# Optimization experiments

Measured on AMD Instinct MI355X. Metric: run time of the kernel, lower is better.

The kernel has to match this reference:

```python
import jax, jax.numpy as jnp
import numpy as np

NEG = -1000000000.0

def setup_inputs() -> dict:
    key = jax.random.key(0)
    k1, k2, k3, k4 = jax.random.split(key, 4)
    B, Sq, Sk, D = 8, 2048, 2048, 1024
    query = jax.random.normal(k1, (B, Sq, D), dtype=jnp.float32)
    memories = jax.random.normal(k2, (B, Sk, D), dtype=jnp.float32)
    mask = jax.random.randint(k3, (B, Sq, Sk), 0, 2).astype(jnp.int32)
    W = jax.random.normal(k4, (D, D), dtype=jnp.float32) * (1.0 / np.sqrt(D))
    b = jnp.zeros((D,), dtype=jnp.float32)
    return {"query": query, "memories": memories, "mask": mask, "W": W, "b": b}

def reference(query, memories, mask, W, b):
    # linear projection: nn.Linear applies x @ W^T + b
    q = jnp.einsum('bsd,od->bso', query, W) + b
    add_mask = (1.0 - mask.astype(q.dtype)) * NEG
    # [B,Sq,Sk] attention logits
    attn_logits = jnp.einsum('bqd,bkd->bqk', q, memories) + add_mask
    attn_weights = jax.nn.softmax(attn_logits, axis=-1)
    attn_outputs = jnp.einsum('bqk,bkd->bqd', attn_weights, memories)
    return attn_outputs
```

## Files before the change

kernel.cpp:

```cpp
#include <hip/hip_runtime.h>


typedef __attribute__((ext_vector_type(8))) _Float16 f16x8;
typedef __attribute__((ext_vector_type(4))) float f32x4;
typedef unsigned short u16;
typedef unsigned int u32;

#define B_ 8
#define SQL 2048
#define SKL 2048
#define DD 1024
#define NEGC -1000000000.0f

static __device__ __forceinline__ u16 f2h(float x) {
  _Float16 h = (_Float16)x;
  return __builtin_bit_cast(u16, h);
}
static __device__ __forceinline__ float h2f(u16 v) {
  return (float)__builtin_bit_cast(_Float16, v);
}
static __device__ __forceinline__ void gload16(const void* g, void* l) {
  __builtin_amdgcn_global_load_lds((const __attribute__((address_space(1))) u32*)g,
                                   (__attribute__((address_space(3))) u32*)l, 16, 0, 0);
}

__global__ __launch_bounds__(256) void cvt16_k(const float* __restrict__ in,
                                               u16* __restrict__ out, long n) {
  long i = ((long)blockIdx.x * 256 + threadIdx.x) * 8;
  long stride = (long)gridDim.x * 256 * 8;
  for (; i < n; i += stride) {
    float4 v0 = *(const float4*)(in + i);
    float4 v1 = *(const float4*)(in + i + 4);
    ushort4 o0 = make_ushort4(f2h(v0.x), f2h(v0.y), f2h(v0.z), f2h(v0.w));
    ushort4 o1 = make_ushort4(f2h(v1.x), f2h(v1.y), f2h(v1.z), f2h(v1.w));
    *(ushort4*)(out + i) = o0;
    *(ushort4*)(out + i + 4) = o1;
  }
}

__global__ __launch_bounds__(256) void split16_k(const float* __restrict__ in,
                                                 u16* __restrict__ hi, u16* __restrict__ lo,
                                                 long n) {
  long i = ((long)blockIdx.x * 256 + threadIdx.x) * 4;
  long stride = (long)gridDim.x * 256 * 4;
  for (; i < n; i += stride) {
    float4 v = *(const float4*)(in + i);
    u16 h0 = f2h(v.x), h1 = f2h(v.y), h2 = f2h(v.z), h3 = f2h(v.w);
    *(ushort4*)(hi + i) = make_ushort4(h0, h1, h2, h3);
    *(ushort4*)(lo + i) = make_ushort4(f2h(v.x - h2f(h0)), f2h(v.y - h2f(h1)),
                                       f2h(v.z - h2f(h2)), f2h(v.w - h2f(h3)));
  }
}

__global__ __launch_bounds__(256) void split_mem16_k(const float* __restrict__ in,
                                                     u16* __restrict__ hi,
                                                     u16* __restrict__ trn) {
  __shared__ u16 t[64][65];
  long bo = (long)blockIdx.z * SKL * DD;
  int r0 = blockIdx.y * 64, c0 = blockIdx.x * 64;
  int tr = threadIdx.x / 16, tc4 = (threadIdx.x % 16) * 4;
#pragma unroll
  for (int i = 0; i < 4; ++i) {
    int r = tr + i * 16;
    long idx = bo + (long)(r0 + r) * DD + c0 + tc4;
    float4 v = *(const float4*)(in + idx);
    u16 h0 = f2h(v.x), h1 = f2h(v.y), h2 = f2h(v.z), h3 = f2h(v.w);
    *(ushort4*)(hi + idx) = make_ushort4(h0, h1, h2, h3);
    t[r][tc4 + 0] = h0; t[r][tc4 + 1] = h1; t[r][tc4 + 2] = h2; t[r][tc4 + 3] = h3;
  }
  __syncthreads();
#pragma unroll
  for (int i = 0; i < 4; ++i) {
    int c = tr + i * 16;
    ushort4 v = make_ushort4(t[tc4 + 0][c], t[tc4 + 1][c], t[tc4 + 2][c], t[tc4 + 3][c]);
    *(ushort4*)(trn + bo + (long)(c0 + c) * SKL + r0 + tc4) = v;
  }
}

template <int TERMS, int OUTMODE, bool BIAS>
__global__ __launch_bounds__(256, 2) void gemm_f16(
    const u16* __restrict__ Ah,
    const u16* __restrict__ Bh, const u16* __restrict__ Bl,
    const float* __restrict__ bias,
    void* __restrict__ C0,
    int N, int K, long batchA, long batchB, long batchC) {
  constexpr int RWB = (TERMS == 2) ? 128 : 64;
  __shared__ u16 lA[128 * 64];
  __shared__ u16 lB[128 * RWB];

  const int nx = gridDim.x;
  int i0 = blockIdx.y * nx + blockIdx.x;
  int nwg = nx * gridDim.y;
  int j = (i0 & 7) * (nwg >> 3) + (i0 >> 3);
  const int bx = j % nx, by = j / nx;

  const int bz = blockIdx.z;
  const u16* pAh = Ah + (long)bz * batchA;
  const u16* pBh = Bh + (long)bz * batchB;
  const u16* pBl = (TERMS == 2) ? Bl : nullptr;

  const int tid = threadIdx.x;
  const int l = tid & 63, w = tid >> 6;
  const int wr = w >> 1, wc = w & 1;
  const long am0 = (long)by * 128;
  const long bn0 = (long)bx * 128;

  f32x4 acc[4][4];
#pragma unroll
  for (int i = 0; i < 4; ++i)
#pragma unroll
    for (int j2 = 0; j2 < 4; ++j2) {
      f32x4 z = {0.f, 0.f, 0.f, 0.f};
      acc[i][j2] = z;
    }

  const int lrow = l & 15, lch = l >> 4;

  for (int k0 = 0; k0 < K; k0 += 64) {
    __syncthreads();
#pragma unroll
    for (int i = 0; i < 4; ++i) {
      int row = i * 32 + (tid >> 3);
      int cc = (tid & 7) ^ (row & 7);
      gload16(pAh + (am0 + row) * K + k0 + cc * 8, &lA[row * 64 + (tid & 7) * 8]);
    }
    if (TERMS == 2) {
#pragma unroll
      for (int i = 0; i < 8; ++i) {
        int row = i * 16 + (tid >> 4);
        int s = tid & 15;
        int cc = s ^ (row & 15);
        const u16* src = (cc < 8) ? (pBh + (bn0 + row) * K + k0 + cc * 8)
                                  : (pBl + (bn0 + row) * K + k0 + (cc - 8) * 8);
        gload16(src, &lB[row * 128 + s * 8]);
      }
    } else {
#pragma unroll
      for (int i = 0; i < 4; ++i) {
        int row = i * 32 + (tid >> 3);
        int cc = (tid & 7) ^ (row & 7);
        gload16(pBh + (bn0 + row) * K + k0 + cc * 8, &lB[row * 64 + (tid & 7) * 8]);
      }
    }
    __syncthreads();

#pragma unroll
    for (int kk = 0; kk < 2; ++kk) {
      if (TERMS == 2) {
        f16x8 ah[4], bh[4], bl_[4];
#pragma unroll
        for (int f = 0; f < 4; ++f) {
          int ra = wr * 64 + f * 16 + lrow;
          int rb = wc * 64 + f * 16 + lrow;
          int c = kk * 4 + lch;
          ah[f] = *(const f16x8*)&lA[ra * 64 + (c ^ (ra & 7)) * 8];
          bh[f] = *(const f16x8*)&lB[rb * 128 + (c ^ (rb & 15)) * 8];
          bl_[f] = *(const f16x8*)&lB[rb * 128 + ((8 + c) ^ (rb & 15)) * 8];
        }
#pragma unroll
        for (int mf = 0; mf < 4; ++mf)
#pragma unroll
          for (int nf = 0; nf < 4; ++nf) {
            acc[mf][nf] = __builtin_amdgcn_mfma_f32_16x16x32_f16(ah[mf], bh[nf], acc[mf][nf], 0, 0, 0);
            acc[mf][nf] = __builtin_amdgcn_mfma_f32_16x16x32_f16(ah[mf], bl_[nf], acc[mf][nf], 0, 0, 0);
          }
      } else {
        f16x8 ah[4], bh[4];
#pragma unroll
        for (int f = 0; f < 4; ++f) {
          int ra = wr * 64 + f * 16 + lrow;
          int rb = wc * 64 + f * 16 + lrow;
          int c = kk * 4 + lch;
          ah[f] = *(const f16x8*)&lA[ra * 64 + (c ^ (ra & 7)) * 8];
          bh[f] = *(const f16x8*)&lB[rb * 64 + (c ^ (rb & 7)) * 8];
        }
#pragma unroll
        for (int mf = 0; mf < 4; ++mf)
#pragma unroll
          for (int nf = 0; nf < 4; ++nf)
            acc[mf][nf] = __builtin_amdgcn_mfma_f32_16x16x32_f16(ah[mf], bh[nf], acc[mf][nf], 0, 0, 0);
      }
    }
  }

#pragma unroll
  for (int mf = 0; mf < 4; ++mf)
#pragma unroll
    for (int nf = 0; nf < 4; ++nf)
#pragma unroll
      for (int r = 0; r < 4; ++r) {
        long row = am0 + wr * 64 + mf * 16 + (l >> 4) * 4 + r;
        long col = bn0 + wc * 64 + nf * 16 + (l & 15);
        float v = acc[mf][nf][r];
        if (BIAS) v += bias[col];
        long idx = (long)bz * batchC + row * N + col;
        if (OUTMODE == 0) ((float*)C0)[idx] = v;
        else              ((u16*)C0)[idx] = f2h(v);
      }
}

__global__ __launch_bounds__(256) void softmax16_k(const float* __restrict__ S,
                                                   const int* __restrict__ M,
                                                   u16* __restrict__ P) {
  long row = blockIdx.x;
  const float* s = S + row * SKL;
  const int* m = M + row * SKL;
  u16* p = P + row * SKL;
  int t = threadIdx.x;
  float x[8];
#pragma unroll
  for (int j = 0; j < 2; ++j) {
    float4 v = *(const float4*)(s + t * 8 + j * 4);
    int4 q = *(const int4*)(m + t * 8 + j * 4);
    x[j * 4 + 0] = q.x ? v.x : v.x + NEGC;
    x[j * 4 + 1] = q.y ? v.y : v.y + NEGC;
    x[j * 4 + 2] = q.z ? v.z : v.z + NEGC;
    x[j * 4 + 3] = q.w ? v.w : v.w + NEGC;
  }
  float mx = x[0];
#pragma unroll
  for (int j = 1; j < 8; ++j) mx = fmaxf(mx, x[j]);
#pragma unroll
  for (int o = 32; o >= 1; o >>= 1) mx = fmaxf(mx, __shfl_xor(mx, o, 64));
  __shared__ float red[8];
  if ((t & 63) == 0) red[t >> 6] = mx;
  __syncthreads();
  mx = fmaxf(fmaxf(red[0], red[1]), fmaxf(red[2], red[3]));
  float e[8], sum = 0.f;
#pragma unroll
  for (int j = 0; j < 8; ++j) { e[j] = __expf(x[j] - mx); sum += e[j]; }
#pragma unroll
  for (int o = 32; o >= 1; o >>= 1) sum += __shfl_xor(sum, o, 64);
  if ((t & 63) == 0) red[4 + (t >> 6)] = sum;
  __syncthreads();
  float inv = 1.f / (red[4] + red[5] + red[6] + red[7]);
  ushort4 o0 = make_ushort4(f2h(e[0] * inv), f2h(e[1] * inv), f2h(e[2] * inv), f2h(e[3] * inv));
  ushort4 o1 = make_ushort4(f2h(e[4] * inv), f2h(e[5] * inv), f2h(e[6] * inv), f2h(e[7] * inv));
  *(ushort4*)(p + t * 8) = o0;
  *(ushort4*)(p + t * 8 + 4) = o1;
}

extern "C" void kernel_launch(void* const* d_in, const int* in_sizes, int n_in,
                              void* d_out, int out_size, void* d_ws, size_t ws_size,
                              hipStream_t stream) {
  const float* query = (const float*)d_in[0];
  const float* mem = (const float*)d_in[1];
  const int* mask = (const int*)d_in[2];
  const float* Wm = (const float*)d_in[3];
  const float* bias = (const float*)d_in[4];
  float* out = (float*)d_out;

  const long nQ = (long)B_ * SQL * DD;
  const long nW = (long)DD * DD;
  const long nS = (long)B_ * SQL * SKL;

  char* ws = (char*)d_ws;
  u16* q16 = (u16*)ws; ws += nQ * 2;
  u16* memh = (u16*)ws; ws += nQ * 2;
  u16* memT = (u16*)ws; ws += nQ * 2;
  u16* q1 = (u16*)ws; ws += nQ * 2;
  u16* wh = (u16*)ws; ws += nW * 2;
  u16* wl = (u16*)ws; ws += nW * 2;
  float* S = (float*)ws; ws += nS * 4;
  u16* P = q16;

  cvt16_k<<<2048, 256, 0, stream>>>(query, q16, nQ);
  split16_k<<<512, 256, 0, stream>>>(Wm, wh, wl, nW);
  split_mem16_k<<<dim3(DD / 64, SKL / 64, B_), 256, 0, stream>>>(mem, memh, memT);

  gemm_f16<2, 1, true><<<dim3(DD / 128, (B_ * SQL) / 128, 1), 256, 0, stream>>>(
      q16, wh, wl, bias, q1, DD, DD, 0, 0, 0);
  gemm_f16<1, 0, false><<<dim3(SKL / 128, SQL / 128, B_), 256, 0, stream>>>(
      q1, memh, nullptr, nullptr, S, SKL, DD,
      (long)SQL * DD, (long)SKL * DD, (long)SQL * SKL);
  softmax16_k<<<B_ * SQL, 256, 0, stream>>>(S, mask, P);
  gemm_f16<1, 0, false><<<dim3(DD / 128, SQL / 128, B_), 256, 0, stream>>>(
      P, memT, nullptr, nullptr, out, DD, SKL,
      (long)SQL * SKL, (long)DD * SKL, (long)SQL * DD);
}
```

Before: 353.9 us.

## Double-buffer LDS tiles in single-term f16 GEMM to overlap loads with MFMA

For the TERMS==1 GEMM variant, LDS tiles are doubled so the next k-tile's global-to-LDS loads are issued before computing the current tile. Partial vmcnt waits and raw s_barrier calls with sched barriers replace the two __syncthreads per iteration. This hides global load latency behind MFMA work. The cost is double the LDS for this variant, which may limit the two-blocks-per-CU occupancy. The two-term path is unchanged.

```diff
diff --git a/kernel.cpp b/kernel.cpp
--- a/kernel.cpp
+++ b/kernel.cpp
@@ -84,9 +84,10 @@
     const float* __restrict__ bias,
     void* __restrict__ C0,
     int N, int K, long batchA, long batchB, long batchC) {
+  constexpr int NBUF = (TERMS == 1) ? 2 : 1;
   constexpr int RWB = (TERMS == 2) ? 128 : 64;
-  __shared__ u16 lA[128 * 64];
-  __shared__ u16 lB[128 * RWB];
+  __shared__ u16 lA[NBUF][128 * 64];
+  __shared__ u16 lB[NBUF][128 * RWB];
 
   const int nx = gridDim.x;
   int i0 = blockIdx.y * nx + blockIdx.x;
@@ -116,15 +117,64 @@
 
   const int lrow = l & 15, lch = l >> 4;
 
-  for (int k0 = 0; k0 < K; k0 += 64) {
-    __syncthreads();
-#pragma unroll
-    for (int i = 0; i < 4; ++i) {
-      int row = i * 32 + (tid >> 3);
-      int cc = (tid & 7) ^ (row & 7);
-      gload16(pAh + (am0 + row) * K + k0 + cc * 8, &lA[row * 64 + (tid & 7) * 8]);
+  if constexpr (TERMS == 1) {
+    auto STAGE = [&](int buf, int k0) {
+#pragma unroll
+      for (int i = 0; i < 4; ++i) {
+        int row = i * 32 + (tid >> 3);
+        int cc = (tid & 7) ^ (row & 7);
+        gload16(pAh + (am0 + row) * K + k0 + cc * 8, &lA[buf][row * 64 + (tid & 7) * 8]);
+        gload16(pBh + (bn0 + row) * K + k0 + cc * 8, &lB[buf][row * 64 + (tid & 7) * 8]);
+      }
+    };
+    auto COMPUTE = [&](int buf) {
+#pragma unroll
+      for (int kk = 0; kk < 2; ++kk) {
+        f16x8 ah[4], bh[4];
+#pragma unroll
+        for (int f = 0; f < 4; ++f) {
+          int ra = wr * 64 + f * 16 + lrow;
+          int rb = wc * 64 + f * 16 + lrow;
+          int c = kk * 4 + lch;
+          ah[f] = *(const f16x8*)&lA[buf][ra * 64 + (c ^ (ra & 7)) * 8];
+          bh[f] = *(const f16x8*)&lB[buf][rb * 64 + (c ^ (rb & 7)) * 8];
+        }
+#pragma unroll
+        for (int mf = 0; mf < 4; ++mf)
+#pragma unroll
+          for (int nf = 0; nf < 4; ++nf)
+            acc[mf][nf] = __builtin_amdgcn_mfma_f32_16x16x32_f16(ah[mf], bh[nf], acc[mf][nf], 0, 0, 0);
+      }
+    };
+
+    const int KITER = K >> 6;
+    STAGE(0, 0);
+    int cur = 0;
+    for (int t = 0; t < KITER; ++t) {
+      if (t + 1 < KITER) {
+        STAGE(cur ^ 1, (t + 1) << 6);
+        asm volatile("s_waitcnt vmcnt(8)" ::: "memory");
+      } else {
+        asm volatile("s_waitcnt vmcnt(0)" ::: "memory");
+      }
+      __builtin_amdgcn_sched_barrier(0);
+      __builtin_amdgcn_s_barrier();
+      __builtin_amdgcn_sched_barrier(0);
+      COMPUTE(cur);
+      asm volatile("s_waitcnt lgkmcnt(0)" ::: "memory");
+      __builtin_amdgcn_sched_barrier(0);
+      __builtin_amdgcn_s_barrier();
+      cur ^= 1;
     }
-    if (TERMS == 2) {
+  } else {
+    for (int k0 = 0; k0 < K; k0 += 64) {
+      __syncthreads();
+#pragma unroll
+      for (int i = 0; i < 4; ++i) {
+        int row = i * 32 + (tid >> 3);
+        int cc = (tid & 7) ^ (row & 7);
+        gload16(pAh + (am0 + row) * K + k0 + cc * 8, &lA[0][row * 64 + (tid & 7) * 8]);
+      }
 #pragma unroll
       for (int i = 0; i < 8; ++i) {
         int row = i * 16 + (tid >> 4);
@@ -132,30 +182,21 @@
         int cc = s ^ (row & 15);
         const u16* src = (cc < 8) ? (pBh + (bn0 + row) * K + k0 + cc * 8)
                                   : (pBl + (bn0 + row) * K + k0 + (cc - 8) * 8);
-        gload16(src, &lB[row * 128 + s * 8]);
-      }
-    } else {
-#pragma unroll
-      for (int i = 0; i < 4; ++i) {
-        int row = i * 32 + (tid >> 3);
-        int cc = (tid & 7) ^ (row & 7);
-        gload16(pBh + (bn0 + row) * K + k0 + cc * 8, &lB[row * 64 + (tid & 7) * 8]);
-      }
-    }
-    __syncthreads();
-
-#pragma unroll
-    for (int kk = 0; kk < 2; ++kk) {
-      if (TERMS == 2) {
+        gload16(src, &lB[0][row * 128 + s * 8]);
+      }
+      __syncthreads();
+
+#pragma unroll
+      for (int kk = 0; kk < 2; ++kk) {
         f16x8 ah[4], bh[4], bl_[4];
 #pragma unroll
         for (int f = 0; f < 4; ++f) {
           int ra = wr * 64 + f * 16 + lrow;
           int rb = wc * 64 + f * 16 + lrow;
           int c = kk * 4 + lch;
-          ah[f] = *(const f16x8*)&lA[ra * 64 + (c ^ (ra & 7)) * 8];
-          bh[f] = *(const f16x8*)&lB[rb * 128 + (c ^ (rb & 15)) * 8];
-          bl_[f] = *(const f16x8*)&lB[rb * 128 + ((8 + c) ^ (rb & 15)) * 8];
+          ah[f] = *(const f16x8*)&lA[0][ra * 64 + (c ^ (ra & 7)) * 8];
+          bh[f] = *(const f16x8*)&lB[0][rb * 128 + (c ^ (rb & 15)) * 8];
+          bl_[f] = *(const f16x8*)&lB[0][rb * 128 + ((8 + c) ^ (rb & 15)) * 8];
         }
 #pragma unroll
         for (int mf = 0; mf < 4; ++mf)
@@ -164,21 +205,6 @@
             acc[mf][nf] = __builtin_amdgcn_mfma_f32_16x16x32_f16(ah[mf], bh[nf], acc[mf][nf], 0, 0, 0);
             acc[mf][nf] = __builtin_amdgcn_mfma_f32_16x16x32_f16(ah[mf], bl_[nf], acc[mf][nf], 0, 0, 0);
           }
-      } else {
-        f16x8 ah[4], bh[4];
-#pragma unroll
-        for (int f = 0; f < 4; ++f) {
-          int ra = wr * 64 + f * 16 + lrow;
-          int rb = wc * 64 + f * 16 + lrow;
-          int c = kk * 4 + lch;
-          ah[f] = *(const f16x8*)&lA[ra * 64 + (c ^ (ra & 7)) * 8];
-          bh[f] = *(const f16x8*)&lB[rb * 64 + (c ^ (rb & 7)) * 8];
-        }
-#pragma unroll
-        for (int mf = 0; mf < 4; ++mf)
-#pragma unroll
-          for (int nf = 0; nf < 4; ++nf)
-            acc[mf][nf] = __builtin_amdgcn_mfma_f32_16x16x32_f16(ah[mf], bh[nf], acc[mf][nf], 0, 0, 0);
       }
     }
   }
```

Result: slower. 362.6 us (+2.5%).
